# Optimization experiments

Measured on AMD Instinct MI355X. Metric: run time of the kernel, lower is better.

Reference implementation:

```python
import jax, jax.numpy as jnp
import numpy as np


def setup_inputs() -> dict:
    key = jax.random.key(0)
    ks = jax.random.split(key, 5)
    B, N, D, K = 128, 50000, 64, 50
    return {
        "basket_emb": jax.random.normal(ks[0], (B, D), dtype=jnp.float32),
        "item_emb": jax.random.normal(ks[1], (N, D), dtype=jnp.float32),
        "Wb": jax.random.normal(ks[2], (D, D), dtype=jnp.float32) / np.sqrt(D),
        "Wi": jax.random.normal(ks[3], (D, D), dtype=jnp.float32) / np.sqrt(D),
        "v": jax.random.normal(ks[4], (D,), dtype=jnp.float32) / np.sqrt(D),
        "k": K,
    }


def reference(basket_emb, item_emb, Wb, Wi, v, k):
    # Additive (Bahdanau-style) scoring: scores[b,n] = v . tanh(Wb@basket_b + Wi@item_n)
    b = basket_emb @ Wb.T            # [B, D]
    i = item_emb @ Wi.T              # [N, D]
    scores = jnp.einsum("bnd,d->bn", jnp.tanh(b[:, None, :] + i[None, :, :]), v)  # [B, N]
    # eval mode: no Gumbel noise (self.training is False for a correctness baseline)
    _, pos_idx = jax.lax.top_k(scores, k)    # top-k highest scores
    _, neg_idx = jax.lax.top_k(-scores, k)   # top-k lowest scores
    return pos_idx, neg_idx
```

## Files before the change

### kernel.cpp

```cpp
#include <hip/hip_runtime.h>

typedef unsigned long long u64;

#define CSC 2.8853900817779268f
#define NBIN 4096
#define CAP  256
#define BT   8
#define MAXJ 16

__device__ __forceinline__ unsigned ord32(float f) {
  unsigned u = __float_as_uint(f);
  return (u & 0x80000000u) ? ~u : (u | 0x80000000u);
}
__device__ __forceinline__ u64 packMax(float f, int n) {
  return ((u64)ord32(f) << 32) | (unsigned)(~(unsigned)n);
}

__global__ void __launch_bounds__(256)
prep_kernel(const float* __restrict__ basket, const float* __restrict__ item,
            const float* __restrict__ Wb, const float* __restrict__ Wi,
            float* __restrict__ ipE, float* __restrict__ bpE,
            int N, int B, int nItemBlk) {
  __shared__ float itS[64][64];
  __shared__ float WT[64][64];
  int tid = threadIdx.x;

  bool isBasket = (blockIdx.x >= nItemBlk);
  const float* src = isBasket ? basket : item;
  const float* W   = isBasket ? Wb : Wi;
  float* dst       = isBasket ? bpE : ipE;
  int r0   = isBasket ? (blockIdx.x - nItemBlk) * 64 : blockIdx.x * 64;
  int rMax = isBasket ? B : N;

  {
    int r = tid & 63, ec = (tid >> 6) * 16;
    const float4* sp = (const float4*)(src + (size_t)(r0 + r) * 64 + ec);
    bool ok = (r0 + r) < rMax;
#pragma unroll
    for (int q = 0; q < 4; ++q) {
      float4 t = ok ? sp[q] : make_float4(0.f, 0.f, 0.f, 0.f);
      itS[ec + 4 * q + 0][r] = t.x;
      itS[ec + 4 * q + 1][r] = t.y;
      itS[ec + 4 * q + 2][r] = t.z;
      itS[ec + 4 * q + 3][r] = t.w;
    }
    const float4* wp = (const float4*)(W + (size_t)r * 64 + ec);
#pragma unroll
    for (int q = 0; q < 4; ++q) {
      float4 t = wp[q];
      WT[ec + 4 * q + 0][r] = t.x;
      WT[ec + 4 * q + 1][r] = t.y;
      WT[ec + 4 * q + 2][r] = t.z;
      WT[ec + 4 * q + 3][r] = t.w;
    }
  }
  __syncthreads();

  int ti = tid & 15, td = tid >> 4;
  float acc[4][4];
#pragma unroll
  for (int i = 0; i < 4; ++i)
#pragma unroll
    for (int j = 0; j < 4; ++j) acc[i][j] = 0.f;

#pragma unroll 8
  for (int e = 0; e < 64; ++e) {
    float4 ri = *(const float4*)&itS[e][4 * ti];
    float4 wd = *(const float4*)&WT[e][4 * td];
    float rr[4] = {ri.x, ri.y, ri.z, ri.w};
    float ww[4] = {wd.x, wd.y, wd.z, wd.w};
#pragma unroll
    for (int i = 0; i < 4; ++i)
#pragma unroll
      for (int j = 0; j < 4; ++j) acc[i][j] = fmaf(rr[i], ww[j], acc[i][j]);
  }

#pragma unroll
  for (int i = 0; i < 4; ++i) {
    int gr = r0 + 4 * ti + i;
    if (gr < rMax) {
      float4 o;
      o.x = __builtin_amdgcn_exp2f(acc[i][0] * CSC);
      o.y = __builtin_amdgcn_exp2f(acc[i][1] * CSC);
      o.z = __builtin_amdgcn_exp2f(acc[i][2] * CSC);
      o.w = __builtin_amdgcn_exp2f(acc[i][3] * CSC);
      *(float4*)(dst + (size_t)gr * 64 + 4 * td) = o;
    }
  }
}

__global__ void __launch_bounds__(256)
scores_kernel(const float* __restrict__ ipE, const float* __restrict__ bpE,
              const float* __restrict__ v, float* __restrict__ scores, int N, int B) {
  int tid = threadIdx.x;
  int b0 = blockIdx.y * BT;
  if (b0 > B - BT) b0 = B - BT;
  int n = blockIdx.x * 256 + tid;
  if (n >= N) return;

  float svf;
  {
    double sv = 0.0;
#pragma unroll
    for (int d = 0; d < 64; ++d) sv += (double)v[d];
    svf = (float)sv;
  }

  float acc[BT];
#pragma unroll
  for (int b = 0; b < BT; ++b) acc[b] = 0.f;

#pragma unroll
  for (int half = 0; half < 2; ++half) {
    float eh[32];
    const float4* p = (const float4*)(ipE + (size_t)n * 64 + half * 32);
#pragma unroll
    for (int i = 0; i < 8; ++i) {
      float4 t = p[i];
      eh[4 * i] = t.x; eh[4 * i + 1] = t.y; eh[4 * i + 2] = t.z; eh[4 * i + 3] = t.w;
    }
    const float* vh = v + half * 32;

#pragma unroll
    for (int b = 0; b < BT; ++b) {
      const float* eb = bpE + (size_t)(b0 + b) * 64 + half * 32;
      float a = acc[b];
#pragma unroll
      for (int h = 0; h < 8; ++h) {
        int q0 = h * 4;
        float x0 = fmaf(eb[q0 + 0], eh[q0 + 0], 1.0f);
        float x1 = fmaf(eb[q0 + 1], eh[q0 + 1], 1.0f);
        float x2 = fmaf(eb[q0 + 2], eh[q0 + 2], 1.0f);
        float x3 = fmaf(eb[q0 + 3], eh[q0 + 3], 1.0f);
        float p01 = x0 * x1, p23 = x2 * x3;
        float den = p01 * p23;
        float n01 = vh[q0 + 0] * x1;
        n01 = fmaf(vh[q0 + 1], x0, n01);
        float n23 = vh[q0 + 2] * x3;
        n23 = fmaf(vh[q0 + 3], x2, n23);
        float num = n01 * p23;
        num = fmaf(n23, p01, num);
        float r = __builtin_amdgcn_rcpf(den);
        a = fmaf(num, r, a);
      }
      acc[b] = a;
    }
  }

#pragma unroll
  for (int b = 0; b < BT; ++b)
    scores[(size_t)(b0 + b) * N + n] = fmaf(-2.0f, acc[b], svf);
}

__global__ void __launch_bounds__(1024)
select_kernel(const float* __restrict__ scores, const float* __restrict__ v,
              int* __restrict__ out, int N, int B, int K) {
  __shared__ int lh[NBIN];
  __shared__ int part[64];
  __shared__ u64 cand[CAP];
  __shared__ int cnt, hHi;
  int tid = threadIdx.x;
  int b = blockIdx.x >> 1, side = blockIdx.x & 1;
  const float* row = scores + (size_t)b * N;
  float sgn = side ? -1.f : 1.f;

  for (int i = tid; i < NBIN; i += 1024) lh[i] = 0;
  if (tid == 0) cnt = 0;

  float R = 0.f;
#pragma unroll
  for (int d = 0; d < 64; ++d) R += fabsf(v[d]);
  float invW = (float)NBIN / (2.f * R);
  __syncthreads();

  float4 v4[MAXJ];
#pragma unroll
  for (int j = 0; j < MAXJ; ++j) {
    int f4 = j * 1024 + tid;
    if (j * 4096 < N && f4 * 4 < N) {
      float4 s4 = *(const float4*)(row + (size_t)f4 * 4);
      s4.x *= sgn; s4.y *= sgn; s4.z *= sgn; s4.w *= sgn;
      v4[j] = s4;
      int n0 = f4 * 4;
      float ss[4] = {s4.x, s4.y, s4.z, s4.w};
#pragma unroll
      for (int c = 0; c < 4; ++c) {
        if (n0 + c < N) {
          int bi = (int)((ss[c] + R) * invW);
          bi = bi < 0 ? 0 : (bi > NBIN - 1 ? NBIN - 1 : bi);
          atomicAdd(&lh[bi], 1);
        }
      }
    }
  }
  __syncthreads();

  if (tid < 64) {
    int s = 0;
    for (int jj = 0; jj < 64; ++jj) s += lh[tid * 64 + jj];
    part[tid] = s;
  }
  __syncthreads();
  if (tid == 0) {
    int cum = 0, c = 63;
    for (; c > 0; --c) { if (cum + part[c] >= K) break; cum += part[c]; }
    int hh = c * 64 + 63;
    for (;; --hh) { cum += lh[hh]; if (cum >= K || hh == 0) break; }
    hHi = hh;
  }
  __syncthreads();
  int hi = hHi;

#pragma unroll
  for (int j = 0; j < MAXJ; ++j) {
    int f4 = j * 1024 + tid;
    if (j * 4096 < N && f4 * 4 < N) {
      int n0 = f4 * 4;
      float ss[4] = {v4[j].x, v4[j].y, v4[j].z, v4[j].w};
#pragma unroll
      for (int c = 0; c < 4; ++c) {
        if (n0 + c < N) {
          float s = ss[c];
          int bi = (int)((s + R) * invW);
          bi = bi < 0 ? 0 : (bi > NBIN - 1 ? NBIN - 1 : bi);
          if (bi >= hi) { int i = atomicAdd(&cnt, 1); if (i < CAP) cand[i] = packMax(s, n0 + c); }
        }
      }
    }
  }
  __syncthreads();

  int tP = cnt < CAP ? cnt : CAP;
  int* dst = out + (side ? (size_t)B * K : 0) + (size_t)b * K;
  for (int i = tid; i < tP; i += 1024) {
    u64 key = cand[i]; int r = 0;
    for (int jj = 0; jj < tP; ++jj) r += (cand[jj] > key);
    if (r < K) dst[r] = (int)(~(unsigned)key);
  }
}

extern "C" void kernel_launch(void* const* d_in, const int* in_sizes, int n_in,
                              void* d_out, int out_size, void* d_ws, size_t ws_size,
                              hipStream_t stream) {
  const float* basket = (const float*)d_in[0];
  const float* item   = (const float*)d_in[1];
  const float* Wb     = (const float*)d_in[2];
  const float* Wi     = (const float*)d_in[3];
  const float* v      = (const float*)d_in[4];
  int D = in_sizes[4];
  int B = in_sizes[0] / D;
  int N = in_sizes[1] / D;
  int K = out_size / (2 * B);

  float* scores = (float*)d_ws;
  float* ipE    = scores + (size_t)B * N;
  float* bpE    = ipE + (size_t)N * 64;

  int nItemBlk = (N + 63) / 64;
  int nBasBlk  = (B + 63) / 64;
  prep_kernel<<<dim3(nItemBlk + nBasBlk), dim3(256), 0, stream>>>(basket, item, Wb, Wi, ipE, bpE, N, B, nItemBlk);

  dim3 gs((N + 255) / 256, (B + BT - 1) / BT);
  scores_kernel<<<gs, dim3(256), 0, stream>>>(ipE, bpE, v, scores, N, B);

  select_kernel<<<dim3(2 * B), dim3(1024), 0, stream>>>(scores, v, (int*)d_out, N, B, K);
}
```

Baseline: 82.62 us.

## Split D across wavefronts in scores kernel with shared-memory reduction

The scores kernel now gives each block 64 items by 32 baskets, with the four wavefronts each handling a 16-wide slice of D for all 32 baskets. Partial sums are staged in shared memory and reduced before the scores are written. This raises per-thread basket reuse of the item slice and cuts per-thread item loads, so each item row is read fewer times across the grid. In exchange it adds a 32KB shared buffer, a block barrier and an extra reduction pass, which may lower occupancy. Basket coefficient loads stay wave-uniform because the slice index goes through readfirstlane.

Measured after the change: 95.08 us. +15.1%, slower.

```diff
diff --git a/kernel.cpp b/kernel.cpp
--- a/kernel.cpp
+++ b/kernel.cpp
@@ -5,7 +5,8 @@
 #define CSC 2.8853900817779268f
 #define NBIN 4096
 #define CAP  256
-#define BT   8
+#define SNB  64
+#define SBB  32
 #define MAXJ 16
 
 __device__ __forceinline__ unsigned ord32(float f) {
@@ -92,11 +93,13 @@
 __global__ void __launch_bounds__(256)
 scores_kernel(const float* __restrict__ ipE, const float* __restrict__ bpE,
               const float* __restrict__ v, float* __restrict__ scores, int N, int B) {
+  __shared__ float part[4][SBB][SNB];
   int tid = threadIdx.x;
-  int b0 = blockIdx.y * BT;
-  if (b0 > B - BT) b0 = B - BT;
-  int n = blockIdx.x * 256 + tid;
-  if (n >= N) return;
+  int ni = tid & 63;
+  int ds = __builtin_amdgcn_readfirstlane(tid >> 6);
+  int n0 = blockIdx.x * SNB;
+  int b0 = blockIdx.y * SBB;
+  int n = n0 + ni;
 
   float svf;
   {
@@ -106,50 +109,59 @@
     svf = (float)sv;
   }
 
-  float acc[BT];
-#pragma unroll
-  for (int b = 0; b < BT; ++b) acc[b] = 0.f;
-
-#pragma unroll
-  for (int half = 0; half < 2; ++half) {
-    float eh[32];
-    const float4* p = (const float4*)(ipE + (size_t)n * 64 + half * 32);
-#pragma unroll
-    for (int i = 0; i < 8; ++i) {
+  float eh[16];
+  if (n < N) {
+    const float4* p = (const float4*)(ipE + (size_t)n * 64 + ds * 16);
+#pragma unroll
+    for (int i = 0; i < 4; ++i) {
       float4 t = p[i];
       eh[4 * i] = t.x; eh[4 * i + 1] = t.y; eh[4 * i + 2] = t.z; eh[4 * i + 3] = t.w;
     }
-    const float* vh = v + half * 32;
-
-#pragma unroll
-    for (int b = 0; b < BT; ++b) {
-      const float* eb = bpE + (size_t)(b0 + b) * 64 + half * 32;
-      float a = acc[b];
-#pragma unroll
-      for (int h = 0; h < 8; ++h) {
-        int q0 = h * 4;
-        float x0 = fmaf(eb[q0 + 0], eh[q0 + 0], 1.0f);
-        float x1 = fmaf(eb[q0 + 1], eh[q0 + 1], 1.0f);
-        float x2 = fmaf(eb[q0 + 2], eh[q0 + 2], 1.0f);
-        float x3 = fmaf(eb[q0 + 3], eh[q0 + 3], 1.0f);
-        float p01 = x0 * x1, p23 = x2 * x3;
-        float den = p01 * p23;
-        float n01 = vh[q0 + 0] * x1;
-        n01 = fmaf(vh[q0 + 1], x0, n01);
-        float n23 = vh[q0 + 2] * x3;
-        n23 = fmaf(vh[q0 + 3], x2, n23);
-        float num = n01 * p23;
-        num = fmaf(n23, p01, num);
-        float r = __builtin_amdgcn_rcpf(den);
-        a = fmaf(num, r, a);
-      }
-      acc[b] = a;
-    }
-  }
-
-#pragma unroll
-  for (int b = 0; b < BT; ++b)
-    scores[(size_t)(b0 + b) * N + n] = fmaf(-2.0f, acc[b], svf);
+  } else {
+#pragma unroll
+    for (int i = 0; i < 16; ++i) eh[i] = 0.f;
+  }
+  const float* vh = v + ds * 16;
+
+  float acc[SBB];
+#pragma unroll
+  for (int b = 0; b < SBB; ++b) {
+    const float* eb = bpE + (size_t)(b0 + b) * 64 + ds * 16;
+    float a = 0.f;
+#pragma unroll
+    for (int h = 0; h < 4; ++h) {
+      int q0 = h * 4;
+      float x0 = fmaf(eb[q0 + 0], eh[q0 + 0], 1.0f);
+      float x1 = fmaf(eb[q0 + 1], eh[q0 + 1], 1.0f);
+      float x2 = fmaf(eb[q0 + 2], eh[q0 + 2], 1.0f);
+      float x3 = fmaf(eb[q0 + 3], eh[q0 + 3], 1.0f);
+      float p01 = x0 * x1, p23 = x2 * x3;
+      float den = p01 * p23;
+      float n01 = vh[q0 + 0] * x1;
+      n01 = fmaf(vh[q0 + 1], x0, n01);
+      float n23 = vh[q0 + 2] * x3;
+      n23 = fmaf(vh[q0 + 3], x2, n23);
+      float num = n01 * p23;
+      num = fmaf(n23, p01, num);
+      float r = __builtin_amdgcn_rcpf(den);
+      a = fmaf(num, r, a);
+    }
+    acc[b] = a;
+  }
+
+#pragma unroll
+  for (int b = 0; b < SBB; ++b) part[ds][b][ni] = acc[b];
+  __syncthreads();
+
+#pragma unroll
+  for (int k = 0; k < 8; ++k) {
+    int pidx = tid + k * 256;
+    int b = pidx >> 6, nn = pidx & 63;
+    if (n0 + nn < N) {
+      float t = ((part[0][b][nn] + part[1][b][nn]) + part[2][b][nn]) + part[3][b][nn];
+      scores[(size_t)(b0 + b) * N + n0 + nn] = fmaf(-2.0f, t, svf);
+    }
+  }
 }
 
 __global__ void __launch_bounds__(1024)
@@ -260,7 +272,7 @@
   int nBasBlk  = (B + 63) / 64;
   prep_kernel<<<dim3(nItemBlk + nBasBlk), dim3(256), 0, stream>>>(basket, item, Wb, Wi, ipE, bpE, N, B, nItemBlk);
 
-  dim3 gs((N + 255) / 256, (B + BT - 1) / BT);
+  dim3 gs((N + SNB - 1) / SNB, (B + SBB - 1) / SBB);
   scores_kernel<<<gs, dim3(256), 0, stream>>>(ipE, bpE, v, scores, N, B);
 
   select_kernel<<<dim3(2 * B), dim3(1024), 0, stream>>>(scores, v, (int*)d_out, N, B, K);
```
